# Kernel tuning notes

Hardware: AMD Instinct MI355X
Metric: run time of the kernel (lower is better)

The kernel has to match this reference:

```python
import jax, jax.numpy as jnp
import numpy as np

NUM_CLASSES = 5
VDIM = 16
IN_CH = 512
B, H, W = 32, 64, 64
LEVEL_OFFSETS = [0, 2, 5, 9]  # flat offsets of levels 1..4 (2,3,4,5 nodes)


def conv1x1(x, w, b):
    # x: [B,C,H,W], w: [O,C], b: [O] -> [B,O,H,W]
    return jnp.einsum('bchw,oc->bohw', x, w) + b[None, :, None, None]


def setup_inputs() -> dict:
    key = jax.random.key(0)
    ks = jax.random.split(key, 8)
    features = jax.random.normal(ks[0], (B, IN_CH, H, W), dtype=jnp.float32)
    # He init (fan_out = out_channels for 1x1 convs), biases zero
    root_w = jax.random.normal(ks[1], (VDIM, IN_CH), dtype=jnp.float32) * np.sqrt(2.0 / VDIM)
    root_b = jnp.zeros((VDIM,), jnp.float32)
    level_w = jax.random.normal(ks[2], (14, VDIM, VDIM), dtype=jnp.float32) * np.sqrt(2.0 / VDIM)
    level_b = jnp.zeros((14, VDIM), jnp.float32)
    m1_w = jax.random.normal(ks[3], (64, VDIM), dtype=jnp.float32) * np.sqrt(2.0 / 64.0)
    m1_b = jnp.zeros((64,), jnp.float32)
    m2_w = jax.random.normal(ks[4], (1, 64), dtype=jnp.float32) * np.sqrt(2.0 / 1.0)
    m2_b = jnp.zeros((1,), jnp.float32)
    return dict(features=features, root_w=root_w, root_b=root_b,
                level_w=level_w, level_b=level_b,
                m1_w=m1_w, m1_b=m1_b, m2_w=m2_w, m2_b=m2_b)


def reference(features, root_w, root_b, level_w, level_b, m1_w, m1_b, m2_w, m2_b):
    b = features.shape[0]
    feats = [conv1x1(features, root_w, root_b)]  # level 0: root, [B,VDIM,H,W]
    for level in range(1, NUM_CLASSES):
        off = LEVEL_OFFSETS[level - 1]
        num_nodes = level + 1
        nxt = []
        for node in range(num_nodes):
            pl = max(0, node - 1)
            pr = min(node, level - 1)
            if pl == pr:
                parent = feats[pl]
            else:
                # L2 norm of GAP-pooled parent vectors; pick larger-norm parent
                ln = jnp.linalg.norm(feats[pl].mean(axis=(2, 3)), axis=1)  # [B]
                rn = jnp.linalg.norm(feats[pr].mean(axis=(2, 3)), axis=1)
                sel = (rn > ln).astype(features.dtype)[:, None, None, None]
                parent = feats[pl] * (1.0 - sel) + feats[pr] * sel
            nxt.append(conv1x1(parent, level_w[off + node], level_b[off + node]))
        feats = nxt
    # leaves: NUM_CLASSES tensors [B,VDIM,H,W]
    leaf_pooled = jnp.stack([f.mean(axis=(2, 3)) for f in feats], axis=1)  # [B,K,VDIM]
    class_logits = jnp.linalg.norm(leaf_pooled, axis=2)                    # [B,K]
    selected_class = jnp.argmax(class_logits, axis=1)                      # [B]
    leaf_stack = jnp.stack(feats, axis=1)                                  # [B,K,VDIM,H,W]
    sel_idx = selected_class[:, None, None, None, None]
    selected_feat = jnp.take_along_axis(leaf_stack, sel_idx, axis=1)[:, 0]  # [B,VDIM,H,W]
    feat_norm = jnp.linalg.norm(selected_feat, axis=1, keepdims=True) + 1e-8
    normalized = selected_feat / feat_norm
    m1 = jax.nn.relu(conv1x1(normalized, m1_w, m1_b))
    m2 = conv1x1(m1, m2_w, m2_b)                 # [B,1,H,W]
    mantissa_raw = m2.mean(axis=(2, 3))[:, 0]    # [B]
    mantissa = jax.nn.sigmoid(mantissa_raw) * 0.75 + 0.75
    return (class_logits, mantissa, selected_class)
```

## Files before the change

### kernel.cpp

```cpp
#include <hip/hip_runtime.h>
#include <math.h>

#define HW 4096
#define NB 32
#define VD 16

#define OFF_M0SUM 0
#define OFF_MSUM  512
#define OFF_M     1024
#define OFF_C     9216
#define OFF_WT    9728
#define OFF_F0    17920

__global__ __launch_bounds__(256) void k_transpose(const float* __restrict__ rw,
                                                   float* __restrict__ wt) {
    int i = blockIdx.x * 256 + threadIdx.x;
    if (i < 512 * VD) {
        int c = i >> 4, o = i & 15;
        wt[i] = rw[o * 512 + c];
    }
}

__global__ __launch_bounds__(128) void k_root(const float* __restrict__ feat,
                                              const float* __restrict__ wt,
                                              const float* __restrict__ rb,
                                              float* __restrict__ f0out,
                                              float* __restrict__ m0sum) {
    const int b  = blockIdx.y;
    const int px = blockIdx.x * 256 + threadIdx.x * 2;
    const float* fp = feat + (size_t)b * 512 * HW + px;

    float2 acc[VD];
#pragma unroll
    for (int o = 0; o < VD; ++o) { float bb = rb[o]; acc[o].x = bb; acc[o].y = bb; }

    for (int c = 0; c < 512; c += 4) {
        float2 f0 = *(const float2*)(fp + (size_t)(c + 0) * HW);
        float2 f1 = *(const float2*)(fp + (size_t)(c + 1) * HW);
        float2 f2 = *(const float2*)(fp + (size_t)(c + 2) * HW);
        float2 f3 = *(const float2*)(fp + (size_t)(c + 3) * HW);
#pragma unroll
        for (int o = 0; o < VD; ++o) {
            float w0 = wt[(c + 0) * VD + o];
            float w1 = wt[(c + 1) * VD + o];
            float w2 = wt[(c + 2) * VD + o];
            float w3 = wt[(c + 3) * VD + o];
            acc[o].x += w0 * f0.x + w1 * f1.x + w2 * f2.x + w3 * f3.x;
            acc[o].y += w0 * f0.y + w1 * f1.y + w2 * f2.y + w3 * f3.y;
        }
    }

    float* op = f0out + (size_t)b * VD * HW + px;
#pragma unroll
    for (int o = 0; o < VD; ++o) *(float2*)(op + (size_t)o * HW) = acc[o];

    __shared__ float red[2][VD];
    const int lane = threadIdx.x & 63, wv = threadIdx.x >> 6;
#pragma unroll
    for (int o = 0; o < VD; ++o) {
        float v = acc[o].x + acc[o].y;
#pragma unroll
        for (int off = 32; off > 0; off >>= 1) v += __shfl_down(v, off);
        if (lane == 0) red[wv][o] = v;
    }
    __syncthreads();
    if (threadIdx.x < VD)
        atomicAdd(m0sum + b * VD + threadIdx.x, red[0][threadIdx.x] + red[1][threadIdx.x]);
}

__global__ __launch_bounds__(64) void k_tree(const float* __restrict__ lw,
                                             const float* __restrict__ lb,
                                             float* __restrict__ ws,
                                             float* __restrict__ out) {
    const int b = blockIdx.x;
    const int t = threadIdx.x;
    __shared__ float lm[15][VD];
    __shared__ float Wst[256];
    __shared__ int   path[5];
    const int Soff[5] = {0, 1, 3, 6, 10};
    const int LOFF[4] = {0, 2, 5, 9};

    if (t < VD) lm[0][t] = ws[OFF_M0SUM + b * VD + t] * (1.0f / HW);
    __syncthreads();

    for (int l = 1; l <= 4; ++l) {
        if (t < VD) {
            for (int n = 0; n <= l; ++n) {
                int pl = (n - 1 < 0) ? 0 : (n - 1);
                int pr = (n < l - 1) ? n : (l - 1);
                const float* A = lm[Soff[l - 1] + pl];
                const float* R = lm[Soff[l - 1] + pr];
                bool takeR = false;
                if (pl != pr) {
                    float ln = 0.f, rn = 0.f;
                    for (int k = 0; k < VD; ++k) { ln += A[k] * A[k]; rn += R[k] * R[k]; }
                    takeR = sqrtf(rn) > sqrtf(ln);
                }
                int widx = LOFF[l - 1] + n;
                float s = lb[widx * VD + t];
                for (int k = 0; k < VD; ++k) {
                    float pk = takeR ? R[k] : A[k];
                    s += lw[(widx * VD + t) * VD + k] * pk;
                }
                lm[Soff[l] + n][t] = s;
            }
        }
        __syncthreads();
    }

    if (t == 0) {
        float best = -1.f; int bi = 0;
        for (int n = 0; n < 5; ++n) {
            float s = 0.f;
            for (int k = 0; k < VD; ++k) { float v = lm[10 + n][k]; s += v * v; }
            float lg = sqrtf(s);
            out[b * 5 + n] = lg;
            if (lg > best) { best = lg; bi = n; }
        }
        out[192 + b] = (float)bi;
        int node = bi;
        for (int l = 4; l >= 1; --l) {
            path[l] = LOFF[l - 1] + node;
            int pl = (node - 1 < 0) ? 0 : (node - 1);
            int pr = (node < l - 1) ? node : (l - 1);
            if (pl == pr) node = pl;
            else {
                float ln = 0.f, rn = 0.f;
                for (int k = 0; k < VD; ++k) {
                    float a = lm[Soff[l - 1] + pl][k], r = lm[Soff[l - 1] + pr][k];
                    ln += a * a; rn += r * r;
                }
                node = (sqrtf(rn) > sqrtf(ln)) ? pr : pl;
            }
        }
    }
    __syncthreads();

    for (int i = t; i < 256; i += 64) Wst[i] = lw[path[1] * 256 + i];
    __syncthreads();
    float Mc[VD], cc[VD];
    if (t < VD) {
        for (int i = 0; i < VD; ++i) Mc[i] = Wst[i * VD + t];
        for (int i = 0; i < VD; ++i) cc[i] = lb[path[1] * VD + i];
    }
    for (int l = 2; l <= 4; ++l) {
        __syncthreads();
        for (int i = t; i < 256; i += 64) Wst[i] = lw[path[l] * 256 + i];
        __syncthreads();
        if (t < VD) {
            float nM[VD], nc[VD];
            for (int i = 0; i < VD; ++i) {
                float sm = 0.f, sc = 0.f;
                for (int k = 0; k < VD; ++k) {
                    float w = Wst[i * VD + k];
                    sm += w * Mc[k]; sc += w * cc[k];
                }
                nM[i] = sm; nc[i] = sc + lb[path[l] * VD + i];
            }
            for (int i = 0; i < VD; ++i) { Mc[i] = nM[i]; cc[i] = nc[i]; }
        }
    }
    if (t < VD) {
        for (int i = 0; i < VD; ++i) ws[OFF_M + b * 256 + i * VD + t] = Mc[i];
        if (t == 0) for (int i = 0; i < VD; ++i) ws[OFF_C + b * VD + i] = cc[i];
    }
}

__global__ __launch_bounds__(256) void k_final(const float* __restrict__ f0g,
                                               const float* __restrict__ Mg,
                                               const float* __restrict__ Cg,
                                               const float* __restrict__ m1w,
                                               const float* __restrict__ m1b,
                                               const float* __restrict__ m2w,
                                               const float* __restrict__ m2b,
                                               float* __restrict__ msum) {
    const int b = blockIdx.y;
    const int t = threadIdx.x;
    __shared__ float sM[256], sc[VD], s1w[1024], s1b[64], s2w[64];
    sM[t] = Mg[b * 256 + t];
    for (int i = t; i < 1024; i += 256) s1w[i] = m1w[i];
    if (t < 64) { s1b[t] = m1b[t]; s2w[t] = m2w[t]; }
    if (t < VD) sc[t] = Cg[b * VD + t];
    __syncthreads();

    const float* fp = f0g + (size_t)b * VD * HW + blockIdx.x * 1024 + t * 4;
    float4 f[VD];
#pragma unroll
    for (int j = 0; j < VD; ++j) f[j] = *(const float4*)(fp + (size_t)j * HW);

    float4 v[VD];
#pragma unroll
    for (int i = 0; i < VD; ++i) {
        float4 s; s.x = s.y = s.z = s.w = sc[i];
#pragma unroll
        for (int j = 0; j < VD; ++j) {
            float w = sM[i * VD + j];
            s.x += w * f[j].x; s.y += w * f[j].y; s.z += w * f[j].z; s.w += w * f[j].w;
        }
        v[i] = s;
    }

    float4 n2; n2.x = n2.y = n2.z = n2.w = 0.f;
#pragma unroll
    for (int i = 0; i < VD; ++i) {
        n2.x += v[i].x * v[i].x; n2.y += v[i].y * v[i].y;
        n2.z += v[i].z * v[i].z; n2.w += v[i].w * v[i].w;
    }
    float4 inv;
    inv.x = 1.f / (sqrtf(n2.x) + 1e-8f); inv.y = 1.f / (sqrtf(n2.y) + 1e-8f);
    inv.z = 1.f / (sqrtf(n2.z) + 1e-8f); inv.w = 1.f / (sqrtf(n2.w) + 1e-8f);
#pragma unroll
    for (int i = 0; i < VD; ++i) {
        v[i].x *= inv.x; v[i].y *= inv.y; v[i].z *= inv.z; v[i].w *= inv.w;
    }

    float mb = m2b[0];
    float4 s2; s2.x = s2.y = s2.z = s2.w = mb;
#pragma unroll 8
    for (int o = 0; o < 64; ++o) {
        float4 h; h.x = h.y = h.z = h.w = s1b[o];
#pragma unroll
        for (int i = 0; i < VD; ++i) {
            float w = s1w[o * VD + i];
            h.x += w * v[i].x; h.y += w * v[i].y; h.z += w * v[i].z; h.w += w * v[i].w;
        }
        h.x = fmaxf(h.x, 0.f); h.y = fmaxf(h.y, 0.f);
        h.z = fmaxf(h.z, 0.f); h.w = fmaxf(h.w, 0.f);
        float w2 = s2w[o];
        s2.x += w2 * h.x; s2.y += w2 * h.y; s2.z += w2 * h.z; s2.w += w2 * h.w;
    }
    float psum = s2.x + s2.y + s2.z + s2.w;

    const int lane = t & 63, wv = t >> 6;
#pragma unroll
    for (int off = 32; off > 0; off >>= 1) psum += __shfl_down(psum, off);
    __shared__ float rs[4];
    if (lane == 0) rs[wv] = psum;
    __syncthreads();
    if (t == 0) atomicAdd(msum + b, rs[0] + rs[1] + rs[2] + rs[3]);
}

__global__ __launch_bounds__(64) void k_mant(const float* __restrict__ msum,
                                             float* __restrict__ out) {
    int b = threadIdx.x;
    if (b < NB) {
        float m = msum[b] * (1.0f / HW);
        out[160 + b] = (1.0f / (1.0f + expf(-m))) * 0.75f + 0.75f;
    }
}

extern "C" void kernel_launch(void* const* d_in, const int* in_sizes, int n_in,
                              void* d_out, int out_size, void* d_ws, size_t ws_size,
                              hipStream_t stream) {
    const float* feat    = (const float*)d_in[0];
    const float* root_w  = (const float*)d_in[1];
    const float* root_b  = (const float*)d_in[2];
    const float* level_w = (const float*)d_in[3];
    const float* level_b = (const float*)d_in[4];
    const float* m1w     = (const float*)d_in[5];
    const float* m1b     = (const float*)d_in[6];
    const float* m2w     = (const float*)d_in[7];
    const float* m2b     = (const float*)d_in[8];
    float* ws  = (float*)d_ws;
    float* out = (float*)d_out;

    hipMemsetAsync(ws, 0, (512 + 32) * sizeof(float), stream);

    k_transpose<<<32, 256, 0, stream>>>(root_w, ws + OFF_WT);
    k_root<<<dim3(16, NB), 128, 0, stream>>>(feat, ws + OFF_WT, root_b,
                                             ws + OFF_F0, ws + OFF_M0SUM);
    k_tree<<<NB, 64, 0, stream>>>(level_w, level_b, ws, out);
    k_final<<<dim3(4, NB), 256, 0, stream>>>(ws + OFF_F0, ws + OFF_M, ws + OFF_C,
                                             m1w, m1b, m2w, m2b, ws + OFF_MSUM);
    k_mant<<<1, 64, 0, stream>>>(ws + OFF_MSUM, out);
}
```

Baseline: 445.4 us.

## Split root conv over input channels with partial outputs summed in final kernel

The root 1x1 conv now splits the 512 input channels into two halves across a new grid dimension, with each thread computing four pixels instead of two. Each thread also loads 64 weights per 4-channel step into registers. The two partial outputs go to separate workspace buffers, and the final kernel sums them on load while processing two pixels per thread across twice as many blocks. This aims to improve memory-level parallelism and per-load width in the bandwidth-bound root conv. In exchange it writes and reads an extra 16-channel partial tensor and raises register pressure.

Result: faster. 420.8 us (-5.5%).

```diff
diff --git a/kernel.cpp b/kernel.cpp
--- a/kernel.cpp
+++ b/kernel.cpp
@@ -10,7 +10,8 @@
 #define OFF_M     1024
 #define OFF_C     9216
 #define OFF_WT    9728
-#define OFF_F0    17920
+#define OFF_P0    17920
+#define OFF_P1    2115072
 
 __global__ __launch_bounds__(256) void k_transpose(const float* __restrict__ rw,
                                                    float* __restrict__ wt) {
@@ -24,41 +25,50 @@
 __global__ __launch_bounds__(128) void k_root(const float* __restrict__ feat,
                                               const float* __restrict__ wt,
                                               const float* __restrict__ rb,
-                                              float* __restrict__ f0out,
+                                              float* __restrict__ pbase,
                                               float* __restrict__ m0sum) {
     const int b  = blockIdx.y;
-    const int px = blockIdx.x * 256 + threadIdx.x * 2;
-    const float* fp = feat + (size_t)b * 512 * HW + px;
-
-    float2 acc[VD];
-#pragma unroll
-    for (int o = 0; o < VD; ++o) { float bb = rb[o]; acc[o].x = bb; acc[o].y = bb; }
-
-    for (int c = 0; c < 512; c += 4) {
-        float2 f0 = *(const float2*)(fp + (size_t)(c + 0) * HW);
-        float2 f1 = *(const float2*)(fp + (size_t)(c + 1) * HW);
-        float2 f2 = *(const float2*)(fp + (size_t)(c + 2) * HW);
-        float2 f3 = *(const float2*)(fp + (size_t)(c + 3) * HW);
+    const int s  = blockIdx.z;
+    const int px = blockIdx.x * 512 + threadIdx.x * 4;
+    const int cb = s * 256;
+    const float* fp = feat + (size_t)b * 512 * HW + (size_t)cb * HW + px;
+
+    float4 acc[VD];
+#pragma unroll
+    for (int o = 0; o < VD; ++o) {
+        float bb = (s == 0) ? rb[o] : 0.0f;
+        acc[o].x = bb; acc[o].y = bb; acc[o].z = bb; acc[o].w = bb;
+    }
+
+    for (int c = 0; c < 256; c += 4) {
+        const float* wrow = wt + (size_t)(cb + c) * VD;
+        float wl[64];
+#pragma unroll
+        for (int k = 0; k < 64; ++k) wl[k] = wrow[k];
+
+        float4 f0 = *(const float4*)(fp + (size_t)(c + 0) * HW);
+        float4 f1 = *(const float4*)(fp + (size_t)(c + 1) * HW);
+        float4 f2 = *(const float4*)(fp + (size_t)(c + 2) * HW);
+        float4 f3 = *(const float4*)(fp + (size_t)(c + 3) * HW);
 #pragma unroll
         for (int o = 0; o < VD; ++o) {
-            float w0 = wt[(c + 0) * VD + o];
-            float w1 = wt[(c + 1) * VD + o];
-            float w2 = wt[(c + 2) * VD + o];
-            float w3 = wt[(c + 3) * VD + o];
+            float w0 = wl[o], w1 = wl[VD + o], w2 = wl[2 * VD + o], w3 = wl[3 * VD + o];
             acc[o].x += w0 * f0.x + w1 * f1.x + w2 * f2.x + w3 * f3.x;
             acc[o].y += w0 * f0.y + w1 * f1.y + w2 * f2.y + w3 * f3.y;
-        }
-    }
-
-    float* op = f0out + (size_t)b * VD * HW + px;
-#pragma unroll
-    for (int o = 0; o < VD; ++o) *(float2*)(op + (size_t)o * HW) = acc[o];
+            acc[o].z += w0 * f0.z + w1 * f1.z + w2 * f2.z + w3 * f3.z;
+            acc[o].w += w0 * f0.w + w1 * f1.w + w2 * f2.w + w3 * f3.w;
+        }
+    }
+
+    float* op = pbase + (size_t)s * 2097152 + (size_t)b * VD * HW + px;
+#pragma unroll
+    for (int o = 0; o < VD; ++o) *(float4*)(op + (size_t)o * HW) = acc[o];
 
     __shared__ float red[2][VD];
     const int lane = threadIdx.x & 63, wv = threadIdx.x >> 6;
 #pragma unroll
     for (int o = 0; o < VD; ++o) {
-        float v = acc[o].x + acc[o].y;
+        float v = acc[o].x + acc[o].y + acc[o].z + acc[o].w;
 #pragma unroll
         for (int off = 32; off > 0; off >>= 1) v += __shfl_down(v, off);
         if (lane == 0) red[wv][o] = v;
@@ -166,7 +176,8 @@
     }
 }
 
-__global__ __launch_bounds__(256) void k_final(const float* __restrict__ f0g,
+__global__ __launch_bounds__(256) void k_final(const float* __restrict__ p0,
+                                               const float* __restrict__ p1,
                                                const float* __restrict__ Mg,
                                                const float* __restrict__ Cg,
                                                const float* __restrict__ m1w,
@@ -183,53 +194,51 @@
     if (t < VD) sc[t] = Cg[b * VD + t];
     __syncthreads();
 
-    const float* fp = f0g + (size_t)b * VD * HW + blockIdx.x * 1024 + t * 4;
-    float4 f[VD];
-#pragma unroll
-    for (int j = 0; j < VD; ++j) f[j] = *(const float4*)(fp + (size_t)j * HW);
-
-    float4 v[VD];
+    const size_t base = (size_t)b * VD * HW + blockIdx.x * 512 + t * 2;
+    float2 f[VD];
+#pragma unroll
+    for (int j = 0; j < VD; ++j) {
+        float2 a = *(const float2*)(p0 + base + (size_t)j * HW);
+        float2 c = *(const float2*)(p1 + base + (size_t)j * HW);
+        f[j].x = a.x + c.x; f[j].y = a.y + c.y;
+    }
+
+    float2 v[VD];
 #pragma unroll
     for (int i = 0; i < VD; ++i) {
-        float4 s; s.x = s.y = s.z = s.w = sc[i];
+        float2 s; s.x = s.y = sc[i];
 #pragma unroll
         for (int j = 0; j < VD; ++j) {
             float w = sM[i * VD + j];
-            s.x += w * f[j].x; s.y += w * f[j].y; s.z += w * f[j].z; s.w += w * f[j].w;
+            s.x += w * f[j].x; s.y += w * f[j].y;
         }
         v[i] = s;
     }
 
-    float4 n2; n2.x = n2.y = n2.z = n2.w = 0.f;
-#pragma unroll
-    for (int i = 0; i < VD; ++i) {
-        n2.x += v[i].x * v[i].x; n2.y += v[i].y * v[i].y;
-        n2.z += v[i].z * v[i].z; n2.w += v[i].w * v[i].w;
-    }
-    float4 inv;
-    inv.x = 1.f / (sqrtf(n2.x) + 1e-8f); inv.y = 1.f / (sqrtf(n2.y) + 1e-8f);
-    inv.z = 1.f / (sqrtf(n2.z) + 1e-8f); inv.w = 1.f / (sqrtf(n2.w) + 1e-8f);
-#pragma unroll
-    for (int i = 0; i < VD; ++i) {
-        v[i].x *= inv.x; v[i].y *= inv.y; v[i].z *= inv.z; v[i].w *= inv.w;
-    }
+    float2 n2; n2.x = n2.y = 0.f;
+#pragma unroll
+    for (int i = 0; i < VD; ++i) { n2.x += v[i].x * v[i].x; n2.y += v[i].y * v[i].y; }
+    float2 inv;
+    inv.x = 1.f / (sqrtf(n2.x) + 1e-8f);
+    inv.y = 1.f / (sqrtf(n2.y) + 1e-8f);
+#pragma unroll
+    for (int i = 0; i < VD; ++i) { v[i].x *= inv.x; v[i].y *= inv.y; }
 
     float mb = m2b[0];
-    float4 s2; s2.x = s2.y = s2.z = s2.w = mb;
+    float2 s2; s2.x = s2.y = mb;
 #pragma unroll 8
     for (int o = 0; o < 64; ++o) {
-        float4 h; h.x = h.y = h.z = h.w = s1b[o];
+        float2 h; h.x = h.y = s1b[o];
 #pragma unroll
         for (int i = 0; i < VD; ++i) {
             float w = s1w[o * VD + i];
-            h.x += w * v[i].x; h.y += w * v[i].y; h.z += w * v[i].z; h.w += w * v[i].w;
+            h.x += w * v[i].x; h.y += w * v[i].y;
         }
         h.x = fmaxf(h.x, 0.f); h.y = fmaxf(h.y, 0.f);
-        h.z = fmaxf(h.z, 0.f); h.w = fmaxf(h.w, 0.f);
         float w2 = s2w[o];
-        s2.x += w2 * h.x; s2.y += w2 * h.y; s2.z += w2 * h.z; s2.w += w2 * h.w;
-    }
-    float psum = s2.x + s2.y + s2.z + s2.w;
+        s2.x += w2 * h.x; s2.y += w2 * h.y;
+    }
+    float psum = s2.x + s2.y;
 
     const int lane = t & 63, wv = t >> 6;
 #pragma unroll
@@ -267,10 +276,11 @@
     hipMemsetAsync(ws, 0, (512 + 32) * sizeof(float), stream);
 
     k_transpose<<<32, 256, 0, stream>>>(root_w, ws + OFF_WT);
-    k_root<<<dim3(16, NB), 128, 0, stream>>>(feat, ws + OFF_WT, root_b,
-                                             ws + OFF_F0, ws + OFF_M0SUM);
+    k_root<<<dim3(8, NB, 2), 128, 0, stream>>>(feat, ws + OFF_WT, root_b,
+                                               ws + OFF_P0, ws + OFF_M0SUM);
     k_tree<<<NB, 64, 0, stream>>>(level_w, level_b, ws, out);
-    k_final<<<dim3(4, NB), 256, 0, stream>>>(ws + OFF_F0, ws + OFF_M, ws + OFF_C,
+    k_final<<<dim3(8, NB), 256, 0, stream>>>(ws + OFF_P0, ws + OFF_P1,
+                                             ws + OFF_M, ws + OFF_C,
                                              m1w, m1b, m2w, m2b, ws + OFF_MSUM);
     k_mant<<<1, 64, 0, stream>>>(ws + OFF_MSUM, out);
 }
```
